# Performance work log

Measured on AMD Instinct MI355X. Metric: run time of the kernel, lower is better.

The kernel has to match this reference:

```python
import jax, jax.numpy as jnp
import numpy as np

DIM_PROBLEM = 8192
DIM_CONTEXT = 512
DIM_HIDDEN = 1024


def setup_inputs() -> dict:
    key = jax.random.key(0)
    ks = jax.random.split(key, 8)
    s = 0.02
    H, C = DIM_HIDDEN, DIM_CONTEXT
    return {
        "context": jax.random.normal(ks[0], (C,), jnp.float32),
        # linear_1: dim_context -> 1
        "W1": jax.random.normal(ks[1], (1, C), jnp.float32) * s,
        "b1": jnp.zeros((1,), jnp.float32),
        # LSTM layer 0 (input dim 1), torch gate order [i, f, g, o]
        "Wih0": jax.random.normal(ks[2], (4 * H, 1), jnp.float32) * s,
        "Whh0": jax.random.normal(ks[3], (4 * H, H), jnp.float32) * s,
        "bih0": jnp.zeros((4 * H,), jnp.float32),
        "bhh0": jnp.zeros((4 * H,), jnp.float32),
        # LSTM layer 1 (input dim H)
        "Wih1": jax.random.normal(ks[4], (4 * H, H), jnp.float32) * s,
        "Whh1": jax.random.normal(ks[5], (4 * H, H), jnp.float32) * s,
        "bih1": jnp.zeros((4 * H,), jnp.float32),
        "bhh1": jnp.zeros((4 * H,), jnp.float32),
        # linear_2: dim_hidden -> 1
        "W2": jax.random.normal(ks[6], (1, H), jnp.float32) * s,
        "b2": jnp.zeros((1,), jnp.float32),
    }


def _lstm_cell(gin, h, c, Whh, b):
    # gin = W_ih @ x (precomputed); torch gate order i, f, g, o
    gates = gin + Whh @ h + b
    i, f, g, o = jnp.split(gates, 4)
    i, f, o = jax.nn.sigmoid(i), jax.nn.sigmoid(f), jax.nn.sigmoid(o)
    g = jnp.tanh(g)
    c = f * c + i * g
    return o * jnp.tanh(c), c


def reference(context, W1, b1, Wih0, Whh0, bih0, bhh0, Wih1, Whh1, bih1, bhh1, W2, b2):
    H = Whh0.shape[1]
    x0 = (W1 @ context + b1)[0]  # linear_1 seeds the first LSTM input (scalar)
    b0 = bih0 + bhh0
    b1g = bih1 + bhh1
    keys = jax.random.split(jax.random.key(42), DIM_PROBLEM)

    def step(carry, k):
        h0, c0, h1, c1, x, logp = carry
        h0, c0 = _lstm_cell(Wih0[:, 0] * x, h0, c0, Whh0, b0)
        h1, c1 = _lstm_cell(Wih1 @ h0, h1, c1, Whh1, b1g)
        p = jax.nn.sigmoid(W2 @ h1 + b2)[0]
        # Bernoulli sample; detached as in the original (.clone().detach(), .item())
        s = jax.lax.stop_gradient(jax.random.bernoulli(k, p).astype(jnp.float32))
        # log of running product  p^s * (1-p)^(1-s)
        logp = logp + s * jnp.log(p) + (1.0 - s) * jnp.log1p(-p)
        return (h0, c0, h1, c1, s, logp), s

    z = jnp.zeros((H,), jnp.float32)
    carry0 = (z, z, z, z, x0, jnp.float32(0.0))
    (_, _, _, _, _, logp), solution = jax.lax.scan(step, carry0, keys)
    return solution, logp
```

## Files before the change

### kernel.cpp

```cpp
#include <hip/hip_runtime.h>
#include <stdint.h>
#include <math.h>


#define H     1024
#define NSTEP 8192
#define NWG   512
#define BLK   64
#define NROW  25

typedef _Float16 h2 __attribute__((ext_vector_type(2)));
typedef _Float16 h8 __attribute__((ext_vector_type(8)));

union U32H2 { uint32_t u; h2 v; };

__device__ __forceinline__ unsigned long long pack_vt(float v0, float v1, uint32_t tag){
  U32H2 p; p.v.x = (_Float16)v0; p.v.y = (_Float16)v1;
  return ((unsigned long long)tag << 32) | (unsigned long long)p.u;
}

__device__ __forceinline__ uint2 tf2x32(uint32_t k0, uint32_t k1, uint32_t x0, uint32_t x1){
  uint32_t k2 = k0 ^ k1 ^ 0x1BD11BDAu;
  x0 += k0; x1 += k1;
#define TFR(r) { x0 += x1; x1 = (x1 << (r)) | (x1 >> (32 - (r))); x1 ^= x0; }
  TFR(13) TFR(15) TFR(26) TFR(6)
  x0 += k1; x1 += k2 + 1u;
  TFR(17) TFR(29) TFR(16) TFR(24)
  x0 += k2; x1 += k0 + 2u;
  TFR(13) TFR(15) TFR(26) TFR(6)
  x0 += k0; x1 += k1 + 3u;
  TFR(17) TFR(29) TFR(16) TFR(24)
  x0 += k1; x1 += k2 + 4u;
  TFR(13) TFR(15) TFR(26) TFR(6)
  x0 += k2; x1 += k0 + 5u;
#undef TFR
  uint2 r; r.x = x0; r.y = x1; return r;
}

__device__ __forceinline__ uint32_t jax_word(uint32_t i){
  return (i < 8192u) ? tf2x32(0u, 42u, i, i + 8192u).x
                     : tf2x32(0u, 42u, i - 8192u, i).y;
}

__device__ __forceinline__ float wred64(float x){
  #pragma unroll
  for(int off = 32; off > 0; off >>= 1) x += __shfl_xor(x, off, 64);
  return x;
}

#if __has_builtin(__builtin_amdgcn_fdot2)
__device__ __forceinline__ float fdot2f(h2 a, h2 b, float c){ return __builtin_amdgcn_fdot2(a, b, c, false); }
#else
__device__ __forceinline__ float fdot2f(h2 a, h2 b, float c){
  return (float)a.x * (float)b.x + (float)a.y * (float)b.y + c;
}
#endif

__device__ __forceinline__ float sigm(float x){
  x = fminf(fmaxf(x, -30.f), 30.f);
  return 1.f / (1.f + __expf(-x));
}
__device__ __forceinline__ float tanh_f(float x){
  x = fminf(fmaxf(x, -15.f), 15.f);
  float e = __expf(2.f * x);
  return (e - 1.f) / (e + 1.f);
}

__device__ __forceinline__ unsigned long long ld_slot(const unsigned long long* p){
  return __hip_atomic_load((unsigned long long*)p, __ATOMIC_RELAXED, __HIP_MEMORY_SCOPE_AGENT);
}

__device__ __forceinline__ void poll_h(const unsigned long long* __restrict__ buf,
                                       uint32_t tag, int lane, h2* hv){
  const unsigned long long* p0 = buf + (lane << 2);
  const unsigned long long* p1 = buf + 256 + (lane << 2);
  unsigned long long pv[8];
  #pragma unroll
  for(int k = 0; k < 4; k++) pv[k]     = ld_slot(p0 + k);
  #pragma unroll
  for(int k = 0; k < 4; k++) pv[4 + k] = ld_slot(p1 + k);
  #pragma unroll
  for(int k = 0; k < 8; k++){
    const unsigned long long* p = (k < 4) ? (p0 + k) : (p1 + (k - 4));
    while((uint32_t)(pv[k] >> 32) != tag){
      __builtin_amdgcn_s_sleep(1);
      pv[k] = ld_slot(p);
    }
  }
  #pragma unroll
  for(int k = 0; k < 8; k++){
    U32H2 u; u.u = (uint32_t)pv[k];
    hv[k] = u.v;
  }
}

__device__ __forceinline__ float row_part(const h2* __restrict__ wrow, int lane, const h2* hv){
  h8 wl = *(const h8*)(wrow + (lane << 2));
  h8 wh = *(const h8*)(wrow + 256 + (lane << 2));
  float a0 = 0.f, a1 = 0.f;
  h2 w;
  w = __builtin_shufflevector(wl, wl, 0, 1); a0 = fdot2f(w, hv[0], a0);
  w = __builtin_shufflevector(wl, wl, 2, 3); a1 = fdot2f(w, hv[1], a1);
  w = __builtin_shufflevector(wl, wl, 4, 5); a0 = fdot2f(w, hv[2], a0);
  w = __builtin_shufflevector(wl, wl, 6, 7); a1 = fdot2f(w, hv[3], a1);
  w = __builtin_shufflevector(wh, wh, 0, 1); a0 = fdot2f(w, hv[4], a0);
  w = __builtin_shufflevector(wh, wh, 2, 3); a1 = fdot2f(w, hv[5], a1);
  w = __builtin_shufflevector(wh, wh, 4, 5); a0 = fdot2f(w, hv[6], a0);
  w = __builtin_shufflevector(wh, wh, 6, 7); a1 = fdot2f(w, hv[7], a1);
  return a0 + a1;
}

__global__ void __launch_bounds__(BLK)
lstm_persist(const float* __restrict__ ctx,  const float* __restrict__ W1p,  const float* __restrict__ b1p,
             const float* __restrict__ Wih0, const float* __restrict__ Whh0,
             const float* __restrict__ bih0, const float* __restrict__ bhh0,
             const float* __restrict__ Wih1, const float* __restrict__ Whh1,
             const float* __restrict__ bih1, const float* __restrict__ bhh1,
             const float* __restrict__ W2p,  const float* __restrict__ b2p,
             float* __restrict__ out,
             unsigned long long* __restrict__ h0buf,
             unsigned long long* __restrict__ h1buf)
{
  __shared__ h2 w[NROW][H/2];

  const int lane = threadIdx.x;
  const int wg   = blockIdx.x;
  const int j0   = wg << 1;

  #pragma unroll 1
  for(int r = 0; r < NROW; r++){
    const float* rowp;
    if(r < 8)      { int g = r & 3,        j = j0 + (r >> 2);        rowp = Wih1 + (size_t)(g*H + j)*H; }
    else if(r < 16){ int rr = r - 8;  int g = rr & 3, j = j0 + (rr >> 2); rowp = Whh0 + (size_t)(g*H + j)*H; }
    else if(r < 24){ int rr = r - 16; int g = rr & 3, j = j0 + (rr >> 2); rowp = Whh1 + (size_t)(g*H + j)*H; }
    else           rowp = W2p;
    const float4* s4 = (const float4*)rowp;
    #pragma unroll
    for(int it = 0; it < 4; it++){
      float4 f = s4[lane + (it << 6)];
      h2 pa; pa.x = (_Float16)f.x; pa.y = (_Float16)f.y;
      h2 pb; pb.x = (_Float16)f.z; pb.y = (_Float16)f.w;
      const int ci = (lane + (it << 6)) << 1;
      w[r][ci] = pa; w[r][ci + 1] = pb;
    }
  }
  __syncthreads();

  float b0g[8], b1g[8], w0g[8];
  #pragma unroll
  for(int e = 0; e < 2; e++){
    const int j = j0 + e;
    #pragma unroll
    for(int g = 0; g < 4; g++){
      b0g[4*e + g] = bih0[g*H + j] + bhh0[g*H + j];
      b1g[4*e + g] = bih1[g*H + j] + bhh1[g*H + j];
      w0g[4*e + g] = Wih0[g*H + j];
    }
  }
  const float b2v = b2p[0];

  float xacc = 0.f;
  for(int c = lane; c < 512; c += 64) xacc += W1p[c] * ctx[c];
  const float x0 = wred64(xacc) + b1p[0];

  float c0[2], c1[2] = {0.f, 0.f}, logp = 0.f;
  float a0[8];
  float a1[8] = {0.f,0.f,0.f,0.f,0.f,0.f,0.f,0.f};

  {
    float h0v[2];
    #pragma unroll
    for(int e = 0; e < 2; e++){
      float gi = sigm (w0g[4*e+0]*x0 + b0g[4*e+0]);
      float gf = sigm (w0g[4*e+1]*x0 + b0g[4*e+1]);
      float gg = tanh_f(w0g[4*e+2]*x0 + b0g[4*e+2]);
      float go = sigm (w0g[4*e+3]*x0 + b0g[4*e+3]);
      c0[e] = gi * gg;
      h0v[e] = go * tanh_f(c0[e]);
    }
    if(lane == 0)
      __hip_atomic_store(&h0buf[wg], pack_vt(h0v[0], h0v[1], 1u),
                         __ATOMIC_RELAXED, __HIP_MEMORY_SCOPE_AGENT);
  }

  h2 hv[8];
  float u = 0.f;

  #pragma unroll 1
  for(int t = 0; t < NSTEP; t++){
    const uint32_t tt = (uint32_t)t;

    poll_h(h0buf, tt + 1u, lane, hv);

    float s1[8];
    #pragma unroll
    for(int r = 0; r < 8; r++) s1[r] = row_part(&w[r][0], lane, hv);
    #pragma unroll
    for(int off = 32; off > 0; off >>= 1){
      #pragma unroll
      for(int r = 0; r < 8; r++) s1[r] += __shfl_xor(s1[r], off, 64);
    }
    {
      float h1v[2];
      #pragma unroll
      for(int e = 0; e < 2; e++){
        float gi = sigm (s1[4*e+0] + a1[4*e+0] + b1g[4*e+0]);
        float gf = sigm (s1[4*e+1] + a1[4*e+1] + b1g[4*e+1]);
        float gg = tanh_f(s1[4*e+2] + a1[4*e+2] + b1g[4*e+2]);
        float go = sigm (s1[4*e+3] + a1[4*e+3] + b1g[4*e+3]);
        c1[e] = gf*c1[e] + gi*gg;
        h1v[e] = go * tanh_f(c1[e]);
      }
      if(lane == 0)
        __hip_atomic_store(&h1buf[wg], pack_vt(h1v[0], h1v[1], tt + 1u),
                           __ATOMIC_RELAXED, __HIP_MEMORY_SCOPE_AGENT);
    }

    {
      const uint32_t kk0 = jax_word(2u*tt), kk1 = jax_word(2u*tt + 1u);
      const uint32_t bits = tf2x32(kk0, kk1, 0u, 0u).x;
      u = __uint_as_float((bits >> 9) | 0x3f800000u) - 1.0f;
    }
    float sa[8];
    #pragma unroll
    for(int r = 0; r < 8; r++) sa[r] = row_part(&w[8 + r][0], lane, hv);
    #pragma unroll
    for(int off = 32; off > 0; off >>= 1){
      #pragma unroll
      for(int r = 0; r < 8; r++) sa[r] += __shfl_xor(sa[r], off, 64);
    }
    #pragma unroll
    for(int r = 0; r < 8; r++) a0[r] = sa[r];

    poll_h(h1buf, tt + 1u, lane, hv);

    float z = row_part(&w[24][0], lane, hv);
    z = wred64(z) + b2v;
    const float p = sigm(z);
    const float s = (u < p) ? 1.f : 0.f;
    logp += s * __logf(p) + (1.f - s) * __logf(1.f - p);
    if(wg == 0 && lane == 0) out[t] = s;
    {
      float h0v[2];
      #pragma unroll
      for(int e = 0; e < 2; e++){
        float gi = sigm (a0[4*e+0] + w0g[4*e+0]*s + b0g[4*e+0]);
        float gf = sigm (a0[4*e+1] + w0g[4*e+1]*s + b0g[4*e+1]);
        float gg = tanh_f(a0[4*e+2] + w0g[4*e+2]*s + b0g[4*e+2]);
        float go = sigm (a0[4*e+3] + w0g[4*e+3]*s + b0g[4*e+3]);
        c0[e] = gf*c0[e] + gi*gg;
        h0v[e] = go * tanh_f(c0[e]);
      }
      if(lane == 0)
        __hip_atomic_store(&h0buf[wg], pack_vt(h0v[0], h0v[1], tt + 2u),
                           __ATOMIC_RELAXED, __HIP_MEMORY_SCOPE_AGENT);
    }

    float sb[8];
    #pragma unroll
    for(int r = 0; r < 8; r++) sb[r] = row_part(&w[16 + r][0], lane, hv);
    #pragma unroll
    for(int off = 32; off > 0; off >>= 1){
      #pragma unroll
      for(int r = 0; r < 8; r++) sb[r] += __shfl_xor(sb[r], off, 64);
    }
    #pragma unroll
    for(int r = 0; r < 8; r++) a1[r] = sb[r];
  }

  if(wg == 0 && lane == 0) out[NSTEP] = logp;
}

extern "C" void kernel_launch(void* const* d_in, const int* in_sizes, int n_in,
                              void* d_out, int out_size, void* d_ws, size_t ws_size,
                              hipStream_t stream){
  unsigned long long* h0buf = (unsigned long long*)d_ws;
  unsigned long long* h1buf = h0buf + 512;
  hipLaunchKernelGGL(lstm_persist, dim3(NWG), dim3(BLK), 0, stream,
    (const float*)d_in[0],  (const float*)d_in[1],  (const float*)d_in[2],
    (const float*)d_in[3],  (const float*)d_in[4],  (const float*)d_in[5],  (const float*)d_in[6],
    (const float*)d_in[7],  (const float*)d_in[8],  (const float*)d_in[9],  (const float*)d_in[10],
    (const float*)d_in[11], (const float*)d_in[12],
    (float*)d_out, h0buf, h1buf);
}
```

Before: 33.34 ms.

## Speculate layer-0 update for both sample values to shorten per-step critical path

Each step now computes the layer-0 LSTM update for both possible Bernoulli outcomes (s=0 and s=1) before the sample is known. Both candidate h0 halves are published in one packed slot, and each workgroup picks the correct half once it has drawn the sample. This takes the h0 exchange off the sequential path behind h1, z and the sample, leaving one cross-workgroup wait on the critical path instead of two. The exchange buffers are double-buffered by step parity, global loads are issued before the matvecs so they overlap, and the threefry uniforms are computed 64 steps at a time and fetched with a shuffle. In exchange it doubles the layer-0 gate math and the exchange traffic. Tags start at 0, so a zeroed or stale workspace could satisfy the first waits too early.

Result: slower. 61.45 ms (+84.3%).

```diff
diff --git a/kernel.cpp b/kernel.cpp
--- a/kernel.cpp
+++ b/kernel.cpp
@@ -11,12 +11,13 @@
 
 typedef _Float16 h2 __attribute__((ext_vector_type(2)));
 typedef _Float16 h8 __attribute__((ext_vector_type(8)));
+typedef unsigned long long u64;
 
 union U32H2 { uint32_t u; h2 v; };
 
-__device__ __forceinline__ unsigned long long pack_vt(float v0, float v1, uint32_t tag){
+__device__ __forceinline__ u64 pack2(float v0, float v1, uint32_t tag){
   U32H2 p; p.v.x = (_Float16)v0; p.v.y = (_Float16)v1;
-  return ((unsigned long long)tag << 32) | (unsigned long long)p.u;
+  return ((u64)tag << 32) | (u64)p.u;
 }
 
 __device__ __forceinline__ uint2 tf2x32(uint32_t k0, uint32_t k1, uint32_t x0, uint32_t x1){
@@ -66,31 +67,60 @@
   return (e - 1.f) / (e + 1.f);
 }
 
-__device__ __forceinline__ unsigned long long ld_slot(const unsigned long long* p){
-  return __hip_atomic_load((unsigned long long*)p, __ATOMIC_RELAXED, __HIP_MEMORY_SCOPE_AGENT);
-}
-
-__device__ __forceinline__ void poll_h(const unsigned long long* __restrict__ buf,
-                                       uint32_t tag, int lane, h2* hv){
-  const unsigned long long* p0 = buf + (lane << 2);
-  const unsigned long long* p1 = buf + 256 + (lane << 2);
-  unsigned long long pv[8];
-  #pragma unroll
-  for(int k = 0; k < 4; k++) pv[k]     = ld_slot(p0 + k);
-  #pragma unroll
-  for(int k = 0; k < 4; k++) pv[4 + k] = ld_slot(p1 + k);
-  #pragma unroll
-  for(int k = 0; k < 8; k++){
-    const unsigned long long* p = (k < 4) ? (p0 + k) : (p1 + (k - 4));
-    while((uint32_t)(pv[k] >> 32) != tag){
-      __builtin_amdgcn_s_sleep(1);
-      pv[k] = ld_slot(p);
-    }
-  }
-  #pragma unroll
-  for(int k = 0; k < 8; k++){
-    U32H2 u; u.u = (uint32_t)pv[k];
-    hv[k] = u.v;
+__device__ __forceinline__ u64 ld_slot(const u64* p){
+  return __hip_atomic_load((u64*)p, __ATOMIC_RELAXED, __HIP_MEMORY_SCOPE_AGENT);
+}
+__device__ __forceinline__ void st_slot(u64* p, u64 v){
+  __hip_atomic_store(p, v, __ATOMIC_RELAXED, __HIP_MEMORY_SCOPE_AGENT);
+}
+
+__device__ __forceinline__ void issue4(const u64* p, u64* pv){
+  #pragma unroll
+  for(int k = 0; k < 4; k++) pv[k] = ld_slot(p + k);
+}
+__device__ __forceinline__ void issue8(const u64* p, u64* pv){
+  #pragma unroll
+  for(int k = 0; k < 8; k++) pv[k] = ld_slot(p + k);
+}
+
+__device__ __forceinline__ void wait8(const u64* p0, const u64* p1, uint32_t tag, u64* pv){
+  for(;;){
+    uint32_t bad = 0;
+    #pragma unroll
+    for(int k = 0; k < 8; k++) bad |= ((uint32_t)(pv[k] >> 32)) ^ tag;
+    if(!bad) break;
+    __builtin_amdgcn_s_sleep(1);
+    #pragma unroll
+    for(int k = 0; k < 4; k++) if(((uint32_t)(pv[k] >> 32)) != tag)     pv[k]     = ld_slot(p0 + k);
+    #pragma unroll
+    for(int k = 0; k < 4; k++) if(((uint32_t)(pv[4+k] >> 32)) != tag)   pv[4+k]   = ld_slot(p1 + k);
+  }
+}
+__device__ __forceinline__ void wait16(const u64* q0, const u64* q1, uint32_t tag, u64* cv){
+  for(;;){
+    uint32_t bad = 0;
+    #pragma unroll
+    for(int k = 0; k < 16; k++) bad |= ((uint32_t)(cv[k] >> 32)) ^ tag;
+    if(!bad) break;
+    __builtin_amdgcn_s_sleep(1);
+    #pragma unroll
+    for(int k = 0; k < 8; k++) if(((uint32_t)(cv[k] >> 32)) != tag)     cv[k]     = ld_slot(q0 + k);
+    #pragma unroll
+    for(int k = 0; k < 8; k++) if(((uint32_t)(cv[8+k] >> 32)) != tag)   cv[8+k]   = ld_slot(q1 + k);
+  }
+}
+
+__device__ __forceinline__ void unpack8(const u64* pv, h2* hv){
+  #pragma unroll
+  for(int k = 0; k < 8; k++){ U32H2 p; p.u = (uint32_t)pv[k]; hv[k] = p.v; }
+}
+
+__device__ __forceinline__ void sel_h0(const u64* cv, uint32_t sh, h2* hv){
+  #pragma unroll
+  for(int m = 0; m < 8; m++){
+    uint32_t lo = (((uint32_t)cv[2*m])     >> sh) & 0xffffu;
+    uint32_t hi = (((uint32_t)cv[2*m + 1]) >> sh) & 0xffffu;
+    U32H2 p; p.u = lo | (hi << 16); hv[m] = p.v;
   }
 }
 
@@ -118,8 +148,8 @@
              const float* __restrict__ bih1, const float* __restrict__ bhh1,
              const float* __restrict__ W2p,  const float* __restrict__ b2p,
              float* __restrict__ out,
-             unsigned long long* __restrict__ h0buf,
-             unsigned long long* __restrict__ h1buf)
+             u64* __restrict__ h1b,
+             u64* __restrict__ cb)
 {
   __shared__ h2 w[NROW][H/2];
 
@@ -130,7 +160,7 @@
   #pragma unroll 1
   for(int r = 0; r < NROW; r++){
     const float* rowp;
-    if(r < 8)      { int g = r & 3,        j = j0 + (r >> 2);        rowp = Wih1 + (size_t)(g*H + j)*H; }
+    if(r < 8)      { int g = r & 3,  j = j0 + (r >> 2);               rowp = Wih1 + (size_t)(g*H + j)*H; }
     else if(r < 16){ int rr = r - 8;  int g = rr & 3, j = j0 + (rr >> 2); rowp = Whh0 + (size_t)(g*H + j)*H; }
     else if(r < 24){ int rr = r - 16; int g = rr & 3, j = j0 + (rr >> 2); rowp = Whh1 + (size_t)(g*H + j)*H; }
     else           rowp = W2p;
@@ -163,38 +193,46 @@
   for(int c = lane; c < 512; c += 64) xacc += W1p[c] * ctx[c];
   const float x0 = wred64(xacc) + b1p[0];
 
-  float c0[2], c1[2] = {0.f, 0.f}, logp = 0.f;
-  float a0[8];
+  float c0v[2], c1v[2] = {0.f, 0.f}, logp = 0.f;
   float a1[8] = {0.f,0.f,0.f,0.f,0.f,0.f,0.f,0.f};
+  float ubatch = 0.f;
 
   {
-    float h0v[2];
+    float h00[2];
     #pragma unroll
     for(int e = 0; e < 2; e++){
       float gi = sigm (w0g[4*e+0]*x0 + b0g[4*e+0]);
-      float gf = sigm (w0g[4*e+1]*x0 + b0g[4*e+1]);
+      float gf = sigm (w0g[4*e+1]*x0 + b0g[4*e+1]);  (void)gf;
       float gg = tanh_f(w0g[4*e+2]*x0 + b0g[4*e+2]);
       float go = sigm (w0g[4*e+3]*x0 + b0g[4*e+3]);
-      c0[e] = gi * gg;
-      h0v[e] = go * tanh_f(c0[e]);
-    }
-    if(lane == 0)
-      __hip_atomic_store(&h0buf[wg], pack_vt(h0v[0], h0v[1], 1u),
-                         __ATOMIC_RELAXED, __HIP_MEMORY_SCOPE_AGENT);
-  }
-
-  h2 hv[8];
-  float u = 0.f;
+      c0v[e] = gi * gg;
+      h00[e] = go * tanh_f(c0v[e]);
+    }
+    if(lane == 0){
+      st_slot(&cb[j0],     pack2(h00[0], h00[0], 0u));
+      st_slot(&cb[j0 + 1], pack2(h00[1], h00[1], 0u));
+    }
+  }
+
+  h2 hv0[8], hv1[8];
+  {
+    const u64* q0 = cb + (lane << 3);
+    const u64* q1 = cb + 512 + (lane << 3);
+    u64 cv[16];
+    issue8(q0, cv); issue8(q1, cv + 8);
+    wait16(q0, q1, 0u, cv);
+    sel_h0(cv, 0u, hv0);
+  }
 
   #pragma unroll 1
   for(int t = 0; t < NSTEP; t++){
     const uint32_t tt = (uint32_t)t;
-
-    poll_h(h0buf, tt + 1u, lane, hv);
+    u64* hb  = h1b + ((t & 1) << 9);
+    u64* cbn = cb  + (((t + 1) & 1) << 10);
 
     float s1[8];
     #pragma unroll
-    for(int r = 0; r < 8; r++) s1[r] = row_part(&w[r][0], lane, hv);
+    for(int r = 0; r < 8; r++) s1[r] = row_part(&w[r][0], lane, hv0);
     #pragma unroll
     for(int off = 32; off > 0; off >>= 1){
       #pragma unroll
@@ -208,64 +246,88 @@
         float gf = sigm (s1[4*e+1] + a1[4*e+1] + b1g[4*e+1]);
         float gg = tanh_f(s1[4*e+2] + a1[4*e+2] + b1g[4*e+2]);
         float go = sigm (s1[4*e+3] + a1[4*e+3] + b1g[4*e+3]);
-        c1[e] = gf*c1[e] + gi*gg;
-        h1v[e] = go * tanh_f(c1[e]);
+        c1v[e] = gf*c1v[e] + gi*gg;
+        h1v[e] = go * tanh_f(c1v[e]);
       }
       if(lane == 0)
-        __hip_atomic_store(&h1buf[wg], pack_vt(h1v[0], h1v[1], tt + 1u),
-                           __ATOMIC_RELAXED, __HIP_MEMORY_SCOPE_AGENT);
-    }
-
+        st_slot(&hb[wg], pack2(h1v[0], h1v[1], tt));
+    }
+
+    const u64* hp0 = hb + (lane << 2);
+    const u64* hp1 = hb + 256 + (lane << 2);
+    u64 pv[8];
+    issue4(hp0, pv); issue4(hp1, pv + 4);
+
+    float a0[8];
+    #pragma unroll
+    for(int r = 0; r < 8; r++) a0[r] = row_part(&w[8 + r][0], lane, hv0);
+    #pragma unroll
+    for(int off = 32; off > 0; off >>= 1){
+      #pragma unroll
+      for(int r = 0; r < 8; r++) a0[r] += __shfl_xor(a0[r], off, 64);
+    }
+
+    float c0c[2][2];
     {
-      const uint32_t kk0 = jax_word(2u*tt), kk1 = jax_word(2u*tt + 1u);
+      float h0c[2][2];
+      #pragma unroll
+      for(int e = 0; e < 2; e++){
+        #pragma unroll
+        for(int sb = 0; sb < 2; sb++){
+          const float sv = (float)sb;
+          float gi = sigm (a0[4*e+0] + w0g[4*e+0]*sv + b0g[4*e+0]);
+          float gf = sigm (a0[4*e+1] + w0g[4*e+1]*sv + b0g[4*e+1]);
+          float gg = tanh_f(a0[4*e+2] + w0g[4*e+2]*sv + b0g[4*e+2]);
+          float go = sigm (a0[4*e+3] + w0g[4*e+3]*sv + b0g[4*e+3]);
+          float cc = gf*c0v[e] + gi*gg;
+          c0c[e][sb] = cc;
+          h0c[e][sb] = go * tanh_f(cc);
+        }
+      }
+      if(lane == 0){
+        st_slot(&cbn[j0],     pack2(h0c[0][0], h0c[0][1], tt + 1u));
+        st_slot(&cbn[j0 + 1], pack2(h0c[1][0], h0c[1][1], tt + 1u));
+      }
+    }
+
+    if((t & 63) == 0){
+      const uint32_t i0 = (uint32_t)t + (uint32_t)lane;
+      const uint32_t kk0 = jax_word(2u*i0), kk1 = jax_word(2u*i0 + 1u);
       const uint32_t bits = tf2x32(kk0, kk1, 0u, 0u).x;
-      u = __uint_as_float((bits >> 9) | 0x3f800000u) - 1.0f;
-    }
-    float sa[8];
-    #pragma unroll
-    for(int r = 0; r < 8; r++) sa[r] = row_part(&w[8 + r][0], lane, hv);
-    #pragma unroll
-    for(int off = 32; off > 0; off >>= 1){
-      #pragma unroll
-      for(int r = 0; r < 8; r++) sa[r] += __shfl_xor(sa[r], off, 64);
-    }
-    #pragma unroll
-    for(int r = 0; r < 8; r++) a0[r] = sa[r];
-
-    poll_h(h1buf, tt + 1u, lane, hv);
-
-    float z = row_part(&w[24][0], lane, hv);
+      ubatch = __uint_as_float((bits >> 9) | 0x3f800000u) - 1.0f;
+    }
+
+    wait8(hp0, hp1, tt, pv);
+    unpack8(pv, hv1);
+
+    const u64* cq0 = cbn + (lane << 3);
+    const u64* cq1 = cbn + 512 + (lane << 3);
+    u64 cv[16];
+    if(t < NSTEP - 1){ issue8(cq0, cv); issue8(cq1, cv + 8); }
+
+    float z = row_part(&w[24][0], lane, hv1);
     z = wred64(z) + b2v;
     const float p = sigm(z);
-    const float s = (u < p) ? 1.f : 0.f;
-    logp += s * __logf(p) + (1.f - s) * __logf(1.f - p);
+    const float u = __shfl(ubatch, t & 63, 64);
+    const bool  sb_ = (u < p);
+    const float s = sb_ ? 1.f : 0.f;
+    logp += sb_ ? __logf(p) : __logf(1.f - p);
     if(wg == 0 && lane == 0) out[t] = s;
-    {
-      float h0v[2];
-      #pragma unroll
-      for(int e = 0; e < 2; e++){
-        float gi = sigm (a0[4*e+0] + w0g[4*e+0]*s + b0g[4*e+0]);
-        float gf = sigm (a0[4*e+1] + w0g[4*e+1]*s + b0g[4*e+1]);
-        float gg = tanh_f(a0[4*e+2] + w0g[4*e+2]*s + b0g[4*e+2]);
-        float go = sigm (a0[4*e+3] + w0g[4*e+3]*s + b0g[4*e+3]);
-        c0[e] = gf*c0[e] + gi*gg;
-        h0v[e] = go * tanh_f(c0[e]);
-      }
-      if(lane == 0)
-        __hip_atomic_store(&h0buf[wg], pack_vt(h0v[0], h0v[1], tt + 2u),
-                           __ATOMIC_RELAXED, __HIP_MEMORY_SCOPE_AGENT);
-    }
-
-    float sb[8];
-    #pragma unroll
-    for(int r = 0; r < 8; r++) sb[r] = row_part(&w[16 + r][0], lane, hv);
+    c0v[0] = sb_ ? c0c[0][1] : c0c[0][0];
+    c0v[1] = sb_ ? c0c[1][1] : c0c[1][0];
+
+    #pragma unroll
+    for(int r = 0; r < 8; r++) a1[r] = row_part(&w[16 + r][0], lane, hv1);
     #pragma unroll
     for(int off = 32; off > 0; off >>= 1){
       #pragma unroll
-      for(int r = 0; r < 8; r++) sb[r] += __shfl_xor(sb[r], off, 64);
-    }
-    #pragma unroll
-    for(int r = 0; r < 8; r++) a1[r] = sb[r];
+      for(int r = 0; r < 8; r++) a1[r] += __shfl_xor(a1[r], off, 64);
+    }
+
+    if(t < NSTEP - 1){
+      wait16(cq0, cq1, tt + 1u, cv);
+      sel_h0(cv, sb_ ? 16u : 0u, hv0);
+    }
   }
 
   if(wg == 0 && lane == 0) out[NSTEP] = logp;
@@ -274,12 +336,12 @@
 extern "C" void kernel_launch(void* const* d_in, const int* in_sizes, int n_in,
                               void* d_out, int out_size, void* d_ws, size_t ws_size,
                               hipStream_t stream){
-  unsigned long long* h0buf = (unsigned long long*)d_ws;
-  unsigned long long* h1buf = h0buf + 512;
+  u64* h1b = (u64*)d_ws;
+  u64* cb  = h1b + 1024;
   hipLaunchKernelGGL(lstm_persist, dim3(NWG), dim3(BLK), 0, stream,
     (const float*)d_in[0],  (const float*)d_in[1],  (const float*)d_in[2],
     (const float*)d_in[3],  (const float*)d_in[4],  (const float*)d_in[5],  (const float*)d_in[6],
     (const float*)d_in[7],  (const float*)d_in[8],  (const float*)d_in[9],  (const float*)d_in[10],
     (const float*)d_in[11], (const float*)d_in[12],
-    (float*)d_out, h0buf, h1buf);
-}
+    (float*)d_out, h1b, cb);
+}
```
